# Kernel tuning notes

Hardware: AMD Instinct MI355X
Metric: run time of the kernel (lower is better)

The kernel has to match this reference:

```python
import jax, jax.numpy as jnp
import numpy as np
from functools import partial

DELTA_B = 30.0
DELTA_H = 30.0
NB = 12  # 360/30
NH = 12
E, H, A, MLP, T = 16, 32, 32, 128, 20


def setup_inputs() -> dict:
    key = jax.random.key(0)
    ks = jax.random.split(key, 32)
    B, N = 512, 32
    inp = {}
    inp['x'] = jax.random.normal(ks[0], (B, N, T, 2), jnp.float32)
    inp['dmat'] = jax.random.uniform(ks[1], (B, N, T, N), jnp.float32) * 10.0
    inp['bmat'] = jax.random.uniform(ks[2], (B, N, T, N), jnp.float32) * 360.0
    inp['hmat'] = jax.random.uniform(ks[3], (B, N, T, N), jnp.float32) * 360.0
    inp['mask'] = jnp.ones((B, N, T), jnp.float32)
    g = lambda k, sh, s=0.1: jax.random.normal(k, sh, jnp.float32) * s
    inp['emb_w'] = g(ks[4], (2, E)); inp['emb_b'] = jnp.zeros((E,), jnp.float32)
    inp['w_ih'] = g(ks[5], (E, 4 * H)); inp['w_hh'] = g(ks[6], (H, 4 * H))
    inp['b_ih'] = jnp.zeros((4 * H,), jnp.float32); inp['b_hh'] = jnp.zeros((4 * H,), jnp.float32)
    inp['enc2att_w'] = g(ks[7], (H, A)); inp['enc2att_b'] = jnp.zeros((A,), jnp.float32)
    inp['domain_tab'] = jnp.full((NB, NH), 5.0, jnp.float32)  # domain_parameter init
    inp['spemb_w'] = g(ks[8], (2 * A, A)); inp['spemb_b'] = jnp.zeros((A,), jnp.float32)
    inp['att2enc_w'] = g(ks[9], (A, H)); inp['att2enc_b'] = jnp.zeros((H,), jnp.float32)
    inp['cls_w1'] = g(ks[10], (T * H, MLP)); inp['cls_b1'] = jnp.zeros((MLP,), jnp.float32)
    inp['cls_w2'] = g(ks[11], (MLP, MLP)); inp['cls_b2'] = jnp.zeros((MLP,), jnp.float32)
    inp['cls_w3'] = g(ks[12], (MLP, 1)); inp['cls_b3'] = jnp.zeros((1,), jnp.float32)
    return inp


def _forward(x, dmat, bmat, hmat, mask, emb_w, emb_b, w_ih, w_hh, b_ih, b_hh,
             enc2att_w, enc2att_b, domain_tab, spemb_w, spemb_b,
             att2enc_w, att2enc_b, cls_w1, cls_b1, cls_w2, cls_b2, cls_w3, cls_b3):
    B, N = x.shape[0], x.shape[1]
    xe = x @ emb_w + emb_b                      # [B,N,T,E]
    # time-major sequences for scan
    seq = (jnp.moveaxis(xe, 2, 0), jnp.moveaxis(dmat, 2, 0), jnp.moveaxis(bmat, 2, 0),
           jnp.moveaxis(hmat, 2, 0), jnp.moveaxis(mask, 2, 0))
    h0 = jnp.zeros((B, N, H), xe.dtype)
    c0 = jnp.zeros((B, N, H), xe.dtype)

    def step(carry, inp):
        h, c = carry
        x_t, d_t, b_t, hd_t, m_t = inp
        gates = x_t @ w_ih + h @ w_hh + (b_ih + b_hh)   # [B,N,4H]
        i, f, g, o = jnp.split(gates, 4, axis=-1)
        c_new = jax.nn.sigmoid(f) * c + jax.nn.sigmoid(i) * jnp.tanh(g)
        h_lstm = jax.nn.sigmoid(o) * jnp.tanh(c_new)
        ha = h_lstm @ enc2att_w + enc2att_b              # enc2att -> [B,N,A]
        # spatial attention: domain value from bearing/heading bins vs distance
        ib = jnp.clip(jnp.floor(b_t / DELTA_B), 0, NB - 1).astype(jnp.int32)
        ih = jnp.clip(jnp.floor(hd_t / DELTA_H), 0, NH - 1).astype(jnp.int32)
        w = jax.nn.relu(domain_tab[ib, ih] - d_t)        # [B,N,N]
        w = w * m_t[:, :, None] * m_t[:, None, :]
        w = w / (w.sum(-1, keepdims=True) + 1e-8)
        att = jnp.einsum('bij,bjd->bid', w, ha)          # neighbor-weighted hidden
        emb = jnp.tanh(jnp.concatenate([ha, att], -1) @ spemb_w + spemb_b)
        h_new = emb @ att2enc_w + att2enc_b              # back to hidden_size
        return (h_new, c_new), h_new

    (_, _), hs = jax.lax.scan(step, (h0, c0), seq)       # hs: [T,B,N,H]
    enc = jnp.moveaxis(hs, 0, 2).reshape(B, N, T * H)
    z = jax.nn.leaky_relu(enc @ cls_w1 + cls_b1, 0.2)
    z = jax.nn.leaky_relu(z @ cls_w2 + cls_b2, 0.2)
    return jax.nn.sigmoid(z @ cls_w3 + cls_b3)           # [B,N,1]


def reference(x, dmat, bmat, hmat, mask, emb_w, emb_b, w_ih, w_hh, b_ih, b_hh,
              enc2att_w, enc2att_b, domain_tab, spemb_w, spemb_b,
              att2enc_w, att2enc_b, cls_w1, cls_b1, cls_w2, cls_b2, cls_w3, cls_b3):
    return _forward(x, dmat, bmat, hmat, mask, emb_w, emb_b, w_ih, w_hh, b_ih, b_hh,
                    enc2att_w, enc2att_b, domain_tab, spemb_w, spemb_b,
                    att2enc_w, att2enc_b, cls_w1, cls_b1, cls_w2, cls_b2, cls_w3, cls_b3)
```

## Files before the change

kernel.cpp:

```cpp
#include <hip/hip_runtime.h>
#include <hip/hip_bf16.h>

#define TD_B 512

typedef __bf16 bf16x8 __attribute__((ext_vector_type(8)));
typedef __bf16 bf16x4 __attribute__((ext_vector_type(4)));
typedef float  f32x4  __attribute__((ext_vector_type(4)));

#define MFMA(a, b, c) __builtin_amdgcn_mfma_f32_16x16x32_bf16((a), (b), (c), 0, 0, 0)

__device__ __forceinline__ float sigf(float x)  { return 1.0f / (1.0f + __expf(-x)); }
__device__ __forceinline__ float tanhf_(float x){ return 2.0f / (1.0f + __expf(-2.0f * x)) - 1.0f; }

extern "C" __global__ void __launch_bounds__(256, 2)
traj_disc_kernel(const float* __restrict__ x, const float* __restrict__ dmat,
                 const float* __restrict__ bmat, const float* __restrict__ hmat,
                 const float* __restrict__ mask,
                 const float* __restrict__ emb_w, const float* __restrict__ emb_b,
                 const float* __restrict__ w_ih, const float* __restrict__ w_hh,
                 const float* __restrict__ b_ih, const float* __restrict__ b_hh,
                 const float* __restrict__ e2a_w, const float* __restrict__ e2a_b,
                 const float* __restrict__ dom,
                 const float* __restrict__ sp_w, const float* __restrict__ sp_b,
                 const float* __restrict__ a2e_w, const float* __restrict__ a2e_b,
                 const float* __restrict__ w1, const float* __restrict__ b1,
                 const float* __restrict__ w2, const float* __restrict__ b2,
                 const float* __restrict__ w3, const float* __restrict__ b3,
                 float* __restrict__ out)
{
    const int b    = blockIdx.x;
    const int tid  = threadIdx.x;
    const int lane = tid & 63;
    const int w    = tid >> 6;
    const int l15  = lane & 15;
    const int lg   = lane >> 4;

    __shared__ __bf16 sAin[32][72];
    __shared__ __bf16 sHl [32][40];
    __shared__ __bf16 sWN [32][40];
    __shared__ __bf16 sHaT[32][40];
    __shared__ __bf16 sEmb[32][40];
    __shared__ __bf16 sPA [32][72];
    __shared__ float  sMaskT[20][36];
    __shared__ float  sDom[144];
    __shared__ __bf16 z1bf[32][136];
    __shared__ __bf16 z2bf[32][136];

    for (int idx = tid; idx < 32 * 72; idx += 256)
        (&sAin[0][0])[idx] = (idx % 72 == 48) ? (__bf16)1.0f : (__bf16)0.0f;
    for (int idx = tid; idx < 640; idx += 256) {
        int tt = idx >> 5, n = idx & 31;
        sMaskT[tt][n] = mask[(b * 32 + n) * 20 + tt];
    }
    if (tid < 144) sDom[tid] = dom[tid];

    const int i0 = tid >> 3, p0 = tid & 7;
    const float ewa0 = emb_w[2 * p0],      ewa1 = emb_w[2 * p0 + 1];
    const float ewb0 = emb_w[16 + 2 * p0], ewb1 = emb_w[16 + 2 * p0 + 1];
    const float eb0  = emb_b[2 * p0],      eb1  = emb_b[2 * p0 + 1];

    bf16x8 Ag[2][2];
    #pragma unroll
    for (int mtl = 0; mtl < 2; ++mtl) {
        int c  = (2 * w + mtl) * 16 + l15;
        int cg = (c & 3) * 32 + (c >> 2);
        #pragma unroll
        for (int kt = 0; kt < 2; ++kt)
            #pragma unroll
            for (int j = 0; j < 8; ++j) {
                int k = kt * 32 + lg * 8 + j;
                float v;
                if (k < 16)       v = w_ih[k * 128 + cg];
                else if (k < 48)  v = w_hh[(k - 16) * 128 + cg];
                else if (k == 48) v = b_ih[cg] + b_hh[cg];
                else              v = 0.0f;
                Ag[mtl][kt][j] = (__bf16)v;
            }
    }
    const int mtw = w >> 1, ntw = w & 1;
    const int cw  = ntw * 16 + l15;
    bf16x8 Be2a, Ba2e, Bsp[2][2];
    #pragma unroll
    for (int j = 0; j < 8; ++j) {
        Be2a[j] = (__bf16)e2a_w[(lg * 8 + j) * 32 + cw];
        Ba2e[j] = (__bf16)a2e_w[(lg * 8 + j) * 32 + cw];
    }
    #pragma unroll
    for (int kt = 0; kt < 2; ++kt)
        #pragma unroll
        for (int nt2 = 0; nt2 < 2; ++nt2)
            #pragma unroll
            for (int j = 0; j < 8; ++j)
                Bsp[kt][nt2][j] = (__bf16)sp_w[(kt * 32 + lg * 8 + j) * 32 + nt2 * 16 + l15];
    const float bEw = e2a_b[cw], bAw = a2e_b[cw];
    const float bS2[2] = { sp_b[l15], sp_b[16 + l15] };

    float cst[2][2] = {{0.f, 0.f}, {0.f, 0.f}};
    f32x4 accZ[2][2] = {};
    bf16x8 Bw1cur[2];

    float4 pdv, pbv, phv; float px0, px1;
    {
        int base = ((b * 32 + i0) * 20 + 0) * 32 + 4 * p0;
        pdv = *(const float4*)(dmat + base);
        pbv = *(const float4*)(bmat + base);
        phv = *(const float4*)(hmat + base);
        int xb = ((b * 32 + i0) * 20 + 0) * 2;
        px0 = x[xb]; px1 = x[xb + 1];
    }
    __syncthreads();

    #pragma unroll 1
    for (int t = 0; t < 20; ++t) {
        {
            float4 dv = pdv, bv = pbv, hv = phv;
            float xx0 = px0, xx1 = px1;
            if (t < 19) {
                int base = ((b * 32 + i0) * 20 + (t + 1)) * 32 + 4 * p0;
                pdv = *(const float4*)(dmat + base);
                pbv = *(const float4*)(bmat + base);
                phv = *(const float4*)(hmat + base);
                int xb = ((b * 32 + i0) * 20 + (t + 1)) * 2;
                px0 = x[xb]; px1 = x[xb + 1];
            }
            float4 mj = *(const float4*)&sMaskT[t][4 * p0];
            float  mi = sMaskT[t][i0];
            float wq[4];
            #pragma unroll
            for (int q = 0; q < 4; ++q) {
                float bq = (&bv.x)[q], hq = (&hv.x)[q];
                int ib = (int)floorf(bq * (1.0f / 30.0f)); ib = ib < 0 ? 0 : (ib > 11 ? 11 : ib);
                int ih = (int)floorf(hq * (1.0f / 30.0f)); ih = ih < 0 ? 0 : (ih > 11 ? 11 : ih);
                float v = sDom[ib * 12 + ih] - (&dv.x)[q];
                v = v > 0.f ? v : 0.f;
                wq[q] = v * (&mj.x)[q];
            }
            float s = wq[0] + wq[1] + wq[2] + wq[3];
            s += __shfl_xor(s, 1); s += __shfl_xor(s, 2); s += __shfl_xor(s, 4);
            float inv = mi / (mi * s + 1e-8f);
            bf16x4 wn4;
            #pragma unroll
            for (int q = 0; q < 4; ++q) wn4[q] = (__bf16)(wq[q] * inv);
            *(bf16x4*)&sWN[i0][4 * p0] = wn4;
            sAin[i0][2 * p0]     = (__bf16)(xx0 * ewa0 + xx1 * ewb0 + eb0);
            sAin[i0][2 * p0 + 1] = (__bf16)(xx0 * ewa1 + xx1 * ewb1 + eb1);
        }
        __syncthreads();

        {
            bf16x8 bxh[2][2];
            #pragma unroll
            for (int nt = 0; nt < 2; ++nt)
                #pragma unroll
                for (int kt = 0; kt < 2; ++kt)
                    bxh[nt][kt] = *(const bf16x8*)&sAin[nt * 16 + l15][kt * 32 + lg * 8];
            if (t >= 1) {
                bf16x8 az[2];
                #pragma unroll
                for (int mt = 0; mt < 2; ++mt)
                    az[mt] = *(const bf16x8*)&sAin[mt * 16 + l15][16 + lg * 8];
                #pragma unroll
                for (int mt = 0; mt < 2; ++mt)
                    #pragma unroll
                    for (int ntp = 0; ntp < 2; ++ntp)
                        accZ[mt][ntp] = MFMA(az[mt], Bw1cur[ntp], accZ[mt][ntp]);
            }
            #pragma unroll
            for (int mtl = 0; mtl < 2; ++mtl)
                #pragma unroll
                for (int nt = 0; nt < 2; ++nt) {
                    f32x4 cc = {0.f, 0.f, 0.f, 0.f};
                    cc = MFMA(Ag[mtl][0], bxh[nt][0], cc);
                    cc = MFMA(Ag[mtl][1], bxh[nt][1], cc);
                    float cn = sigf(cc[1]) * cst[mtl][nt] + sigf(cc[0]) * tanhf_(cc[2]);
                    cst[mtl][nt] = cn;
                    sHl[nt * 16 + l15][4 * (2 * w + mtl) + lg] = (__bf16)(sigf(cc[3]) * tanhf_(cn));
                }
            #pragma unroll
            for (int ntp = 0; ntp < 2; ++ntp) {
                int c = (2 * w + ntp) * 16 + l15;
                #pragma unroll
                for (int j = 0; j < 8; ++j)
                    Bw1cur[ntp][j] = (__bf16)w1[(t * 32 + lg * 8 + j) * 128 + c];
            }
        }
        __syncthreads();

        {
            #pragma unroll
            for (int mt = 0; mt < 2; ++mt) {
                bf16x8 a = *(const bf16x8*)&sHl[mt * 16 + l15][lg * 8];
                f32x4 cc = {0.f, 0.f, 0.f, 0.f};
                cc = MFMA(a, Be2a, cc);
                bf16x4 tv;
                #pragma unroll
                for (int q = 0; q < 4; ++q) {
                    float v = cc[q] + bEw;
                    tv[q] = (__bf16)v;
                    sPA[mt * 16 + 4 * lg + q][cw] = (__bf16)v;
                }
                *(bf16x4*)&sHaT[cw][mt * 16 + 4 * lg] = tv;
            }
            bf16x8 aW = *(const bf16x8*)&sWN [mtw * 16 + l15][lg * 8];
            bf16x8 bT = *(const bf16x8*)&sHaT[ntw * 16 + l15][lg * 8];
            f32x4 cc = {0.f, 0.f, 0.f, 0.f};
            cc = MFMA(aW, bT, cc);
            #pragma unroll
            for (int q = 0; q < 4; ++q)
                sPA[mtw * 16 + 4 * lg + q][32 + cw] = (__bf16)cc[q];
        }
        __syncthreads();

        {
            bf16x8 a0 = *(const bf16x8*)&sPA[mtw * 16 + l15][lg * 8];
            bf16x8 a1 = *(const bf16x8*)&sPA[mtw * 16 + l15][32 + lg * 8];
            #pragma unroll
            for (int nt2 = 0; nt2 < 2; ++nt2) {
                f32x4 cc = {0.f, 0.f, 0.f, 0.f};
                cc = MFMA(a0, Bsp[0][nt2], cc);
                cc = MFMA(a1, Bsp[1][nt2], cc);
                #pragma unroll
                for (int q = 0; q < 4; ++q)
                    sEmb[mtw * 16 + 4 * lg + q][nt2 * 16 + l15] = (__bf16)tanhf_(cc[q] + bS2[nt2]);
            }
            bf16x8 ae = *(const bf16x8*)&sEmb[mtw * 16 + l15][lg * 8];
            f32x4 cf = {0.f, 0.f, 0.f, 0.f};
            cf = MFMA(ae, Ba2e, cf);
            #pragma unroll
            for (int q = 0; q < 4; ++q)
                sAin[mtw * 16 + 4 * lg + q][16 + cw] = (__bf16)(cf[q] + bAw);
        }
    }

    __syncthreads();
    {
        bf16x8 az[2];
        #pragma unroll
        for (int mt = 0; mt < 2; ++mt)
            az[mt] = *(const bf16x8*)&sAin[mt * 16 + l15][16 + lg * 8];
        #pragma unroll
        for (int mt = 0; mt < 2; ++mt)
            #pragma unroll
            for (int ntp = 0; ntp < 2; ++ntp)
                accZ[mt][ntp] = MFMA(az[mt], Bw1cur[ntp], accZ[mt][ntp]);
    }
    #pragma unroll
    for (int mt = 0; mt < 2; ++mt)
        #pragma unroll
        for (int ntp = 0; ntp < 2; ++ntp) {
            int c = (2 * w + ntp) * 16 + l15;
            float bias = b1[c];
            #pragma unroll
            for (int q = 0; q < 4; ++q) {
                float v = accZ[mt][ntp][q] + bias;
                v = v > 0.f ? v : 0.2f * v;
                z1bf[mt * 16 + 4 * lg + q][c] = (__bf16)v;
            }
        }
    __syncthreads();

    {
        f32x4 c2[2][2] = {};
        #pragma unroll
        for (int kt = 0; kt < 4; ++kt) {
            bf16x8 a[2];
            #pragma unroll
            for (int mt = 0; mt < 2; ++mt)
                a[mt] = *(const bf16x8*)&z1bf[mt * 16 + l15][kt * 32 + lg * 8];
            bf16x8 bb[2];
            #pragma unroll
            for (int ntp = 0; ntp < 2; ++ntp) {
                int c = (2 * w + ntp) * 16 + l15;
                #pragma unroll
                for (int j = 0; j < 8; ++j)
                    bb[ntp][j] = (__bf16)w2[(kt * 32 + lg * 8 + j) * 128 + c];
            }
            #pragma unroll
            for (int mt = 0; mt < 2; ++mt)
                #pragma unroll
                for (int ntp = 0; ntp < 2; ++ntp)
                    c2[mt][ntp] = MFMA(a[mt], bb[ntp], c2[mt][ntp]);
        }
        #pragma unroll
        for (int mt = 0; mt < 2; ++mt)
            #pragma unroll
            for (int ntp = 0; ntp < 2; ++ntp) {
                int c = (2 * w + ntp) * 16 + l15;
                float bias = b2[c];
                #pragma unroll
                for (int q = 0; q < 4; ++q) {
                    float v = c2[mt][ntp][q] + bias;
                    v = v > 0.f ? v : 0.2f * v;
                    z2bf[mt * 16 + 4 * lg + q][c] = (__bf16)v;
                }
            }
    }
    __syncthreads();

    {
        int n = tid >> 3, kg = tid & 7;
        bf16x8 v0 = *(const bf16x8*)&z2bf[n][kg * 16];
        bf16x8 v1 = *(const bf16x8*)&z2bf[n][kg * 16 + 8];
        float s = 0.f;
        #pragma unroll
        for (int j = 0; j < 8; ++j)
            s += (float)v0[j] * w3[kg * 16 + j] + (float)v1[j] * w3[kg * 16 + 8 + j];
        s += __shfl_xor(s, 1); s += __shfl_xor(s, 2); s += __shfl_xor(s, 4);
        if (kg == 0) out[b * 32 + n] = sigf(s + b3[0]);
    }
}

extern "C" void kernel_launch(void* const* d_in, const int* in_sizes, int n_in,
                              void* d_out, int out_size, void* d_ws, size_t ws_size,
                              hipStream_t stream) {
    (void)in_sizes; (void)n_in; (void)d_ws; (void)ws_size; (void)out_size;
    const float* x     = (const float*)d_in[0];
    const float* dmat  = (const float*)d_in[1];
    const float* bmat  = (const float*)d_in[2];
    const float* hmat  = (const float*)d_in[3];
    const float* mask  = (const float*)d_in[4];
    const float* emb_w = (const float*)d_in[5];
    const float* emb_b = (const float*)d_in[6];
    const float* w_ih  = (const float*)d_in[7];
    const float* w_hh  = (const float*)d_in[8];
    const float* b_ih  = (const float*)d_in[9];
    const float* b_hh  = (const float*)d_in[10];
    const float* e2a_w = (const float*)d_in[11];
    const float* e2a_b = (const float*)d_in[12];
    const float* dom   = (const float*)d_in[13];
    const float* sp_w  = (const float*)d_in[14];
    const float* sp_b  = (const float*)d_in[15];
    const float* a2e_w = (const float*)d_in[16];
    const float* a2e_b = (const float*)d_in[17];
    const float* w1    = (const float*)d_in[18];
    const float* b1    = (const float*)d_in[19];
    const float* w2    = (const float*)d_in[20];
    const float* b2    = (const float*)d_in[21];
    const float* w3    = (const float*)d_in[22];
    const float* b3    = (const float*)d_in[23];
    float* out = (float*)d_out;

    traj_disc_kernel<<<dim3(TD_B), dim3(256), 0, stream>>>(
        x, dmat, bmat, hmat, mask, emb_w, emb_b, w_ih, w_hh, b_ih, b_hh,
        e2a_w, e2a_b, dom, sp_w, sp_b, a2e_w, a2e_b,
        w1, b1, w2, b2, w3, b3, out);
}
```

Before: 77.90 us.

## Double block size to 512 threads and split LSTM and MLP work across eight waves

Raises the block from 256 to 512 threads (eight waves) and gives each wave one 16-column slice of the LSTM gate matmul and the cls_w1/cls_w2 accumulations, instead of two slices per wave. The per-step input preparation is split so the first 256 threads compute the attention weights while the other 256 load x and build the embedding. The aim is to shorten the serial per-timestep critical path by spreading MFMA and transcendental work over more waves. In exchange the per-step barriers cover twice as many threads, and the middle attention section, not shown, may leave the extra waves idle, adding to register and occupancy pressure.

```diff
diff --git a/kernel.cpp b/kernel.cpp
--- a/kernel.cpp
+++ b/kernel.cpp
@@ -12,7 +12,7 @@
 __device__ __forceinline__ float sigf(float x)  { return 1.0f / (1.0f + __expf(-x)); }
 __device__ __forceinline__ float tanhf_(float x){ return 2.0f / (1.0f + __expf(-2.0f * x)) - 1.0f; }
 
-extern "C" __global__ void __launch_bounds__(256, 2)
+extern "C" __global__ void __launch_bounds__(512, 4)
 traj_disc_kernel(const float* __restrict__ x, const float* __restrict__ dmat,
                  const float* __restrict__ bmat, const float* __restrict__ hmat,
                  const float* __restrict__ mask,
@@ -46,23 +46,23 @@
     __shared__ __bf16 z1bf[32][136];
     __shared__ __bf16 z2bf[32][136];
 
-    for (int idx = tid; idx < 32 * 72; idx += 256)
+    for (int idx = tid; idx < 32 * 72; idx += 512)
         (&sAin[0][0])[idx] = (idx % 72 == 48) ? (__bf16)1.0f : (__bf16)0.0f;
-    for (int idx = tid; idx < 640; idx += 256) {
+    for (int idx = tid; idx < 640; idx += 512) {
         int tt = idx >> 5, n = idx & 31;
         sMaskT[tt][n] = mask[(b * 32 + n) * 20 + tt];
     }
     if (tid < 144) sDom[tid] = dom[tid];
 
     const int i0 = tid >> 3, p0 = tid & 7;
+    const int rA = i0 & 31;
     const float ewa0 = emb_w[2 * p0],      ewa1 = emb_w[2 * p0 + 1];
     const float ewb0 = emb_w[16 + 2 * p0], ewb1 = emb_w[16 + 2 * p0 + 1];
     const float eb0  = emb_b[2 * p0],      eb1  = emb_b[2 * p0 + 1];
 
-    bf16x8 Ag[2][2];
-    #pragma unroll
-    for (int mtl = 0; mtl < 2; ++mtl) {
-        int c  = (2 * w + mtl) * 16 + l15;
+    bf16x8 Ag[2];
+    {
+        int c  = 16 * w + l15;
         int cg = (c & 3) * 32 + (c >> 2);
         #pragma unroll
         for (int kt = 0; kt < 2; ++kt)
@@ -74,10 +74,11 @@
                 else if (k < 48)  v = w_hh[(k - 16) * 128 + cg];
                 else if (k == 48) v = b_ih[cg] + b_hh[cg];
                 else              v = 0.0f;
-                Ag[mtl][kt][j] = (__bf16)v;
-            }
-    }
-    const int mtw = w >> 1, ntw = w & 1;
+                Ag[kt][j] = (__bf16)v;
+            }
+    }
+    const int wr  = w & 3;
+    const int mtw = wr >> 1, ntw = wr & 1;
     const int cw  = ntw * 16 + l15;
     bf16x8 Be2a, Ba2e, Bsp[2][2];
     #pragma unroll
@@ -95,33 +96,32 @@
     const float bEw = e2a_b[cw], bAw = a2e_b[cw];
     const float bS2[2] = { sp_b[l15], sp_b[16 + l15] };
 
-    float cst[2][2] = {{0.f, 0.f}, {0.f, 0.f}};
-    f32x4 accZ[2][2] = {};
-    bf16x8 Bw1cur[2];
+    float cst[2] = {0.f, 0.f};
+    f32x4 accZ[2] = {};
+    bf16x8 Bw1cur;
+    const int c1 = 16 * w + l15;
 
     float4 pdv, pbv, phv; float px0, px1;
-    {
+    if (tid < 256) {
         int base = ((b * 32 + i0) * 20 + 0) * 32 + 4 * p0;
         pdv = *(const float4*)(dmat + base);
         pbv = *(const float4*)(bmat + base);
         phv = *(const float4*)(hmat + base);
-        int xb = ((b * 32 + i0) * 20 + 0) * 2;
+    } else {
+        int xb = ((b * 32 + rA) * 20 + 0) * 2;
         px0 = x[xb]; px1 = x[xb + 1];
     }
     __syncthreads();
 
     #pragma unroll 1
     for (int t = 0; t < 20; ++t) {
-        {
+        if (tid < 256) {
             float4 dv = pdv, bv = pbv, hv = phv;
-            float xx0 = px0, xx1 = px1;
             if (t < 19) {
                 int base = ((b * 32 + i0) * 20 + (t + 1)) * 32 + 4 * p0;
                 pdv = *(const float4*)(dmat + base);
                 pbv = *(const float4*)(bmat + base);
                 phv = *(const float4*)(hmat + base);
-                int xb = ((b * 32 + i0) * 20 + (t + 1)) * 2;
-                px0 = x[xb]; px1 = x[xb + 1];
             }
             float4 mj = *(const float4*)&sMaskT[t][4 * p0];
             float  mi = sMaskT[t][i0];
@@ -142,8 +142,14 @@
             #pragma unroll
             for (int q = 0; q < 4; ++q) wn4[q] = (__bf16)(wq[q] * inv);
             *(bf16x4*)&sWN[i0][4 * p0] = wn4;
-            sAin[i0][2 * p0]     = (__bf16)(xx0 * ewa0 + xx1 * ewb0 + eb0);
-            sAin[i0][2 * p0 + 1] = (__bf16)(xx0 * ewa1 + xx1 * ewb1 + eb1);
+        } else {
+            float xx0 = px0, xx1 = px1;
+            if (t < 19) {
+                int xb = ((b * 32 + rA) * 20 + (t + 1)) * 2;
+                px0 = x[xb]; px1 = x[xb + 1];
+            }
+            sAin[rA][2 * p0]     = (__bf16)(xx0 * ewa0 + xx1 * ewb0 + eb0);
+            sAin[rA][2 * p0 + 1] = (__bf16)(xx0 * ewa1 + xx1 * ewb1 + eb1);
         }
         __syncthreads();
 
@@ -155,34 +161,24 @@
                 for (int kt = 0; kt < 2; ++kt)
                     bxh[nt][kt] = *(const bf16x8*)&sAin[nt * 16 + l15][kt * 32 + lg * 8];
             if (t >= 1) {
-                bf16x8 az[2];
                 #pragma unroll
-                for (int mt = 0; mt < 2; ++mt)
-                    az[mt] = *(const bf16x8*)&sAin[mt * 16 + l15][16 + lg * 8];
-                #pragma unroll
-                for (int mt = 0; mt < 2; ++mt)
-                    #pragma unroll
-                    for (int ntp = 0; ntp < 2; ++ntp)
-                        accZ[mt][ntp] = MFMA(az[mt], Bw1cur[ntp], accZ[mt][ntp]);
-            }
-            #pragma unroll
-            for (int mtl = 0; mtl < 2; ++mtl)
-                #pragma unroll
-                for (int nt = 0; nt < 2; ++nt) {
-                    f32x4 cc = {0.f, 0.f, 0.f, 0.f};
-                    cc = MFMA(Ag[mtl][0], bxh[nt][0], cc);
-                    cc = MFMA(Ag[mtl][1], bxh[nt][1], cc);
-                    float cn = sigf(cc[1]) * cst[mtl][nt] + sigf(cc[0]) * tanhf_(cc[2]);
-                    cst[mtl][nt] = cn;
-                    sHl[nt * 16 + l15][4 * (2 * w + mtl) + lg] = (__bf16)(sigf(cc[3]) * tanhf_(cn));
+                for (int mt = 0; mt < 2; ++mt) {
+                    bf16x8 az = *(const bf16x8*)&sAin[mt * 16 + l15][16 + lg * 8];
+                    accZ[mt] = MFMA(az, Bw1cur, accZ[mt]);
                 }
-            #pragma unroll
-            for (int ntp = 0; ntp < 2; ++ntp) {
-                int c = (2 * w + ntp) * 16 + l15;
-                #pragma unroll
-                for (int j = 0; j < 8; ++j)
-                    Bw1cur[ntp][j] = (__bf16)w1[(t * 32 + lg * 8 + j) * 128 + c];
-            }
+            }
+            #pragma unroll
+            for (int nt = 0; nt < 2; ++nt) {
+                f32x4 cc = {0.f, 0.f, 0.f, 0.f};
+                cc = MFMA(Ag[0], bxh[nt][0], cc);
+                cc = MFMA(Ag[1], bxh[nt][1], cc);
+                float cn = sigf(cc[1]) * cst[nt] + sigf(cc[0]) * tanhf_(cc[2]);
+                cst[nt] = cn;
+                sHl[nt * 16 + l15][4 * w + lg] = (__bf16)(sigf(cc[3]) * tanhf_(cn));
+            }
+            #pragma unroll
+            for (int j = 0; j < 8; ++j)
+                Bw1cur[j] = (__bf16)w1[(t * 32 + lg * 8 + j) * 128 + c1];
         }
         __syncthreads();
 
@@ -233,79 +229,59 @@
     }
 
     __syncthreads();
+    #pragma unroll
+    for (int mt = 0; mt < 2; ++mt) {
+        bf16x8 az = *(const bf16x8*)&sAin[mt * 16 + l15][16 + lg * 8];
+        accZ[mt] = MFMA(az, Bw1cur, accZ[mt]);
+    }
     {
-        bf16x8 az[2];
+        float bias = b1[c1];
         #pragma unroll
         for (int mt = 0; mt < 2; ++mt)
-            az[mt] = *(const bf16x8*)&sAin[mt * 16 + l15][16 + lg * 8];
+            #pragma unroll
+            for (int q = 0; q < 4; ++q) {
+                float v = accZ[mt][q] + bias;
+                v = v > 0.f ? v : 0.2f * v;
+                z1bf[mt * 16 + 4 * lg + q][c1] = (__bf16)v;
+            }
+    }
+    __syncthreads();
+
+    {
+        f32x4 c2z[2] = {};
+        #pragma unroll
+        for (int kt = 0; kt < 4; ++kt) {
+            bf16x8 bw2;
+            #pragma unroll
+            for (int j = 0; j < 8; ++j)
+                bw2[j] = (__bf16)w2[(kt * 32 + lg * 8 + j) * 128 + c1];
+            #pragma unroll
+            for (int mt = 0; mt < 2; ++mt) {
+                bf16x8 a = *(const bf16x8*)&z1bf[mt * 16 + l15][kt * 32 + lg * 8];
+                c2z[mt] = MFMA(a, bw2, c2z[mt]);
+            }
+        }
+        float bias = b2[c1];
         #pragma unroll
         for (int mt = 0; mt < 2; ++mt)
             #pragma unroll
-            for (int ntp = 0; ntp < 2; ++ntp)
-                accZ[mt][ntp] = MFMA(az[mt], Bw1cur[ntp], accZ[mt][ntp]);
-    }
-    #pragma unroll
-    for (int mt = 0; mt < 2; ++mt)
-        #pragma unroll
-        for (int ntp = 0; ntp < 2; ++ntp) {
-            int c = (2 * w + ntp) * 16 + l15;
-            float bias = b1[c];
-            #pragma unroll
             for (int q = 0; q < 4; ++q) {
-                float v = accZ[mt][ntp][q] + bias;
+                float v = c2z[mt][q] + bias;
                 v = v > 0.f ? v : 0.2f * v;
-                z1bf[mt * 16 + 4 * lg + q][c] = (__bf16)v;
-            }
-        }
+                z2bf[mt * 16 + 4 * lg + q][c1] = (__bf16)v;
+            }
+    }
     __syncthreads();
 
     {
-        f32x4 c2[2][2] = {};
-        #pragma unroll
-        for (int kt = 0; kt < 4; ++kt) {
-            bf16x8 a[2];
-            #pragma unroll
-            for (int mt = 0; mt < 2; ++mt)
-                a[mt] = *(const bf16x8*)&z1bf[mt * 16 + l15][kt * 32 + lg * 8];
-            bf16x8 bb[2];
-            #pragma unroll
-            for (int ntp = 0; ntp < 2; ++ntp) {
-                int c = (2 * w + ntp) * 16 + l15;
-                #pragma unroll
-                for (int j = 0; j < 8; ++j)
-                    bb[ntp][j] = (__bf16)w2[(kt * 32 + lg * 8 + j) * 128 + c];
-            }
-            #pragma unroll
-            for (int mt = 0; mt < 2; ++mt)
-                #pragma unroll
-                for (int ntp = 0; ntp < 2; ++ntp)
-                    c2[mt][ntp] = MFMA(a[mt], bb[ntp], c2[mt][ntp]);
-        }
-        #pragma unroll
-        for (int mt = 0; mt < 2; ++mt)
-            #pragma unroll
-            for (int ntp = 0; ntp < 2; ++ntp) {
-                int c = (2 * w + ntp) * 16 + l15;
-                float bias = b2[c];
-                #pragma unroll
-                for (int q = 0; q < 4; ++q) {
-                    float v = c2[mt][ntp][q] + bias;
-                    v = v > 0.f ? v : 0.2f * v;
-                    z2bf[mt * 16 + 4 * lg + q][c] = (__bf16)v;
-                }
-            }
-    }
-    __syncthreads();
-
-    {
-        int n = tid >> 3, kg = tid & 7;
-        bf16x8 v0 = *(const bf16x8*)&z2bf[n][kg * 16];
-        bf16x8 v1 = *(const bf16x8*)&z2bf[n][kg * 16 + 8];
+        int n = tid >> 4, kg = tid & 15;
+        bf16x8 v0 = *(const bf16x8*)&z2bf[n][kg * 8];
         float s = 0.f;
         #pragma unroll
         for (int j = 0; j < 8; ++j)
-            s += (float)v0[j] * w3[kg * 16 + j] + (float)v1[j] * w3[kg * 16 + 8 + j];
-        s += __shfl_xor(s, 1); s += __shfl_xor(s, 2); s += __shfl_xor(s, 4);
+            s += (float)v0[j] * w3[kg * 8 + j];
+        s += __shfl_xor(s, 1); s += __shfl_xor(s, 2);
+        s += __shfl_xor(s, 4); s += __shfl_xor(s, 8);
         if (kg == 0) out[b * 32 + n] = sigf(s + b3[0]);
     }
 }
@@ -340,7 +316,7 @@
     const float* b3    = (const float*)d_in[23];
     float* out = (float*)d_out;
 
-    traj_disc_kernel<<<dim3(TD_B), dim3(256), 0, stream>>>(
+    traj_disc_kernel<<<dim3(TD_B), dim3(512), 0, stream>>>(
         x, dmat, bmat, hmat, mask, emb_w, emb_b, w_ih, w_hh, b_ih, b_hh,
         e2a_w, e2a_b, dom, sp_w, sp_b, a2e_w, a2e_b,
         w1, b1, w2, b2, w3, b3, out);
```

New measurement: 92.87 us. +19.2%, slower.
